# Performance work log

Measured on AMD Instinct MI355X. Metric: run time of the kernel, lower is better.

Reference implementation:

```python
import jax, jax.numpy as jnp
import numpy as np
from jax.scipy.special import ndtri

D = 1024
BITS = 4
K = 2 ** BITS
N = 4096


def _rotation_matrix(d, seed):
    # Haar-distributed random orthogonal matrix via QR with sign fix,
    # matching generate_rotation_matrix in the torch source.
    g = np.random.default_rng(seed).standard_normal((d, d)).astype(np.float32)
    Q, R = np.linalg.qr(g)
    s = np.sign(np.diag(R))
    s[s == 0] = 1.0
    return jnp.asarray((Q * s[None, :]).astype(np.float32))


def _lloyd_max_centroids(k):
    # Per-coordinate scalar codebook for a standard Gaussian (Lloyd-Max init
    # via inverse-CDF midpoints), analogous to LloydMaxCodebook.centroids [K].
    probs = (jnp.arange(k, dtype=jnp.float32) + 0.5) / k
    return ndtri(probs).astype(jnp.float32)


def setup_inputs() -> dict:
    key = jax.random.key(0)
    x = jax.random.normal(key, (N, D), dtype=jnp.float32)
    Pi = _rotation_matrix(D, seed=42)          # [d, d]
    centroids = _lloyd_max_centroids(K)        # [K]
    return {"x": x, "Pi": Pi, "centroids": centroids}


def reference(x, Pi, centroids):
    # rotate: y = x @ Pi^T
    y = x @ Pi.T                               # [N, d]
    # per-coordinate nearest-centroid argmin over K
    diffs = jnp.abs(y[..., None] - centroids)  # [N, d, K]
    indices = jnp.argmin(diffs, axis=-1)       # [N, d] int
    # dequantize: gather centroids, then unrotate x_hat = y_hat @ Pi
    y_hat = centroids[indices]                 # [N, d]
    x_hat = y_hat @ Pi                         # [N, d]
    return x_hat, indices
```

## Files before the change

### kernel.cpp

```cpp
#include <hip/hip_runtime.h>
#include <hip/hip_bf16.h>

#define TQ_D   1024
#define TQ_KC  16
#define MERGE_K 512
#define TQ_TOL  1.0e-4f
#define LCAP    1024

typedef __attribute__((ext_vector_type(8))) short bf16x8;
typedef __attribute__((ext_vector_type(4))) float f32x4;

__device__ __forceinline__ unsigned short f2bf(float f) {
    union { __hip_bfloat16 h; unsigned short s; } u;
    u.h = __float2bfloat16(f);
    return u.s;
}
__device__ __forceinline__ float bf2f(unsigned short s) {
    union { unsigned int u; float f; } v;
    v.u = (unsigned int)s << 16;
    return v.f;
}

__global__ __launch_bounds__(512)
void tq_rq_mfma(const float* __restrict__ X,
                const float* __restrict__ Pi,
                const float* __restrict__ Cent,
                float* __restrict__ OutIdx,
                unsigned* __restrict__ Counter,
                unsigned* __restrict__ List,
                unsigned cap)
{
    __shared__ unsigned short XhS[128][40];
    __shared__ unsigned short XlS[128][40];
    __shared__ unsigned short PhS[64][40];
    __shared__ unsigned short PlS[64][40];
    __shared__ unsigned lcount;
    __shared__ unsigned gbase;
    __shared__ unsigned llist[LCAP];

    const int tid  = threadIdx.x;
    const int lane = tid & 63;
    const int wv   = tid >> 6;
    const int m0 = blockIdx.y * 128;
    const int n0 = blockIdx.x * 64;
    const int wr = (wv >> 1) * 32;
    const int wc = (wv & 1) * 32;
    const int l15 = lane & 15;
    const int k8  = (lane >> 4) * 8;

    const int srow = tid >> 2;
    const int scol = (tid & 3) * 8;
    const int brow = tid >> 3;
    const int bcol = (tid & 7) * 4;

    const float* aP = X  + (size_t)(m0 + srow) * TQ_D + scol;
    const float* bP = Pi + (size_t)(n0 + brow) * TQ_D + bcol;

    if (tid == 0) lcount = 0;

    f32x4 acc[2][2];
#pragma unroll
    for (int i = 0; i < 2; ++i)
#pragma unroll
        for (int j = 0; j < 2; ++j)
#pragma unroll
            for (int r = 0; r < 4; ++r) acc[i][j][r] = 0.0f;

    float4 va[2], vb;
#pragma unroll
    for (int q = 0; q < 2; ++q) va[q] = *(const float4*)(aP + 4 * q);
    vb = *(const float4*)(bP);

#pragma unroll
    for (int q = 0; q < 2; ++q) {
        ushort4 ah, al;
        const float* fa = (const float*)&va[q];
        ah.x = f2bf(fa[0]); al.x = f2bf(fa[0] - bf2f(ah.x));
        ah.y = f2bf(fa[1]); al.y = f2bf(fa[1] - bf2f(ah.y));
        ah.z = f2bf(fa[2]); al.z = f2bf(fa[2] - bf2f(ah.z));
        ah.w = f2bf(fa[3]); al.w = f2bf(fa[3] - bf2f(ah.w));
        *(ushort4*)&XhS[srow][scol + 4 * q] = ah;
        *(ushort4*)&XlS[srow][scol + 4 * q] = al;
    }
    {
        ushort4 bh, bl;
        const float* fb = (const float*)&vb;
        bh.x = f2bf(fb[0]); bl.x = f2bf(fb[0] - bf2f(bh.x));
        bh.y = f2bf(fb[1]); bl.y = f2bf(fb[1] - bf2f(bh.y));
        bh.z = f2bf(fb[2]); bl.z = f2bf(fb[2] - bf2f(bh.z));
        bh.w = f2bf(fb[3]); bl.w = f2bf(fb[3] - bf2f(bh.w));
        *(ushort4*)&PhS[brow][bcol] = bh;
        *(ushort4*)&PlS[brow][bcol] = bl;
    }
    __syncthreads();

    for (int kt = 0; kt < 32; ++kt) {
        const bool more = (kt + 1) < 32;
        if (more) {
            const float* ap = aP + (kt + 1) * 32;
            const float* bp = bP + (kt + 1) * 32;
#pragma unroll
            for (int q = 0; q < 2; ++q) va[q] = *(const float4*)(ap + 4 * q);
            vb = *(const float4*)(bp);
        }

        bf16x8 afh[2], afl[2], bfh[2], bfl[2];
#pragma unroll
        for (int i = 0; i < 2; ++i) {
            afh[i] = *(const bf16x8*)&XhS[wr + i * 16 + l15][k8];
            afl[i] = *(const bf16x8*)&XlS[wr + i * 16 + l15][k8];
        }
#pragma unroll
        for (int j = 0; j < 2; ++j) {
            bfh[j] = *(const bf16x8*)&PhS[wc + j * 16 + l15][k8];
            bfl[j] = *(const bf16x8*)&PlS[wc + j * 16 + l15][k8];
        }

#pragma unroll
        for (int i = 0; i < 2; ++i)
#pragma unroll
            for (int j = 0; j < 2; ++j) {
                acc[i][j] = __builtin_amdgcn_mfma_f32_16x16x32_bf16(
                    afh[i], bfh[j], acc[i][j], 0, 0, 0);
                acc[i][j] = __builtin_amdgcn_mfma_f32_16x16x32_bf16(
                    afl[i], bfh[j], acc[i][j], 0, 0, 0);
                acc[i][j] = __builtin_amdgcn_mfma_f32_16x16x32_bf16(
                    afh[i], bfl[j], acc[i][j], 0, 0, 0);
                acc[i][j] = __builtin_amdgcn_mfma_f32_16x16x32_bf16(
                    afl[i], bfl[j], acc[i][j], 0, 0, 0);
            }

        if (more) {
            __syncthreads();
#pragma unroll
            for (int q = 0; q < 2; ++q) {
                ushort4 ah, al;
                const float* fa = (const float*)&va[q];
                ah.x = f2bf(fa[0]); al.x = f2bf(fa[0] - bf2f(ah.x));
                ah.y = f2bf(fa[1]); al.y = f2bf(fa[1] - bf2f(ah.y));
                ah.z = f2bf(fa[2]); al.z = f2bf(fa[2] - bf2f(ah.z));
                ah.w = f2bf(fa[3]); al.w = f2bf(fa[3] - bf2f(ah.w));
                *(ushort4*)&XhS[srow][scol + 4 * q] = ah;
                *(ushort4*)&XlS[srow][scol + 4 * q] = al;
            }
            {
                ushort4 bh, bl;
                const float* fb = (const float*)&vb;
                bh.x = f2bf(fb[0]); bl.x = f2bf(fb[0] - bf2f(bh.x));
                bh.y = f2bf(fb[1]); bl.y = f2bf(fb[1] - bf2f(bh.y));
                bh.z = f2bf(fb[2]); bl.z = f2bf(fb[2] - bf2f(bh.z));
                bh.w = f2bf(fb[3]); bl.w = f2bf(fb[3] - bf2f(bh.w));
                *(ushort4*)&PhS[brow][bcol] = bh;
                *(ushort4*)&PlS[brow][bcol] = bl;
            }
            __syncthreads();
        }
    }

    float c[TQ_KC];
#pragma unroll
    for (int q = 0; q < TQ_KC; ++q) c[q] = Cent[q];

#pragma unroll
    for (int i = 0; i < 2; ++i)
#pragma unroll
        for (int j = 0; j < 2; ++j)
#pragma unroll
            for (int r = 0; r < 4; ++r) {
                const int row = m0 + wr + i * 16 + (lane >> 4) * 4 + r;
                const int col = n0 + wc + j * 16 + l15;
                const float y = acc[i][j][r];
                int best = 0;
                float bd = fabsf(y - c[0]);
#pragma unroll
                for (int q = 1; q < TQ_KC; ++q) {
                    const float d = fabsf(y - c[q]);
                    if (d < bd) { bd = d; best = q; }
                }
                float dist = 1e30f;
#pragma unroll
                for (int q = 0; q < TQ_KC - 1; ++q) {
                    const float mid = 0.5f * (c[q] + c[q + 1]);
                    dist = fminf(dist, fabsf(y - mid));
                }
                if (dist < TQ_TOL) {
                    const unsigned id = ((unsigned)row << 10) | (unsigned)col;
                    const unsigned ls = atomicAdd(&lcount, 1u);
                    if (ls < LCAP) {
                        llist[ls] = id;
                    } else {
                        const unsigned gs = atomicAdd(Counter, 1u);
                        if (gs < cap) List[gs] = id;
                    }
                }
                OutIdx[(size_t)row * TQ_D + col] = (float)best;
            }

    __syncthreads();
    if (tid == 0) {
        const unsigned cnt = min(lcount, (unsigned)LCAP);
        gbase = (cnt > 0) ? atomicAdd(Counter, cnt) : 0u;
    }
    __syncthreads();
    const unsigned cnt = min(lcount, (unsigned)LCAP);
    for (unsigned s = tid; s < cnt; s += 512) {
        const unsigned g = gbase + s;
        if (g < cap) List[g] = llist[s];
    }
}

__global__ __launch_bounds__(256)
void tq_fixup_lds(const float* __restrict__ X,
                  const float* __restrict__ Pi,
                  const float* __restrict__ Cent,
                  float* __restrict__ OutIdx,
                  const unsigned* __restrict__ Counter,
                  const unsigned* __restrict__ List,
                  unsigned cap)
{
    __shared__ float Rows[8][2][1024];
    __shared__ float part[8][2];
    __shared__ unsigned ids[8];

    const int tid = threadIdx.x;
    const unsigned count = min(*Counter, cap);

    for (unsigned base = blockIdx.x * 8; base < count; base += gridDim.x * 8) {
        const unsigned nsus = min(8u, count - base);

        if (tid < 8) ids[tid] = (tid < nsus) ? List[base + tid] : 0u;
        __syncthreads();

#pragma unroll
        for (int q = 0; q < 16; ++q) {
            const int lin = q * 256 + tid;
            const int sus = lin >> 9;
            const int rowsel = (lin >> 8) & 1;
            const int f4 = lin & 255;
            if ((unsigned)sus < nsus) {
                const unsigned id = ids[sus];
                const int m = id >> 10;
                const int n = id & (TQ_D - 1);
                const float* src = rowsel ? (Pi + (size_t)n * TQ_D)
                                          : (X + (size_t)m * TQ_D);
                *(float4*)&Rows[sus][rowsel][f4 * 4] =
                    *(const float4*)(src + f4 * 4);
            }
        }
        __syncthreads();

        if (tid < 16 && (unsigned)(tid >> 1) < nsus) {
            const int sus = tid >> 1;
            const int p = tid & 1;
            const int kb = p * MERGE_K;
            float a = 0.0f;
            for (int k = 0; k < MERGE_K; k += 4) {
                const float4 xa = *(const float4*)&Rows[sus][0][kb + k];
                const float4 pa = *(const float4*)&Rows[sus][1][kb + k];
                a = fmaf(xa.x, pa.x, a);
                a = fmaf(xa.y, pa.y, a);
                a = fmaf(xa.z, pa.z, a);
                a = fmaf(xa.w, pa.w, a);
            }
            part[sus][p] = a;
        }
        __syncthreads();

        if (tid < (int)nsus) {
            const float y = part[tid][0] + part[tid][1];
            float c[TQ_KC];
#pragma unroll
            for (int q = 0; q < TQ_KC; ++q) c[q] = Cent[q];
            int best = 0;
            float bd = fabsf(y - c[0]);
#pragma unroll
            for (int q = 1; q < TQ_KC; ++q) {
                const float d = fabsf(y - c[q]);
                if (d < bd) { bd = d; best = q; }
            }
            const unsigned id = ids[tid];
            OutIdx[(size_t)(id >> 10) * TQ_D + (id & (TQ_D - 1))] = (float)best;
        }
        __syncthreads();
    }
}

__global__ __launch_bounds__(256)
void tq_dq_mfma(const float* __restrict__ IdxF,
                const float* __restrict__ Pi,
                const float* __restrict__ Cent,
                float* __restrict__ Xhat)
{
    __shared__ unsigned short Ys[128][40];
    __shared__ unsigned short Ps[128][40];
    __shared__ unsigned short csb[TQ_KC];

    const int tid  = threadIdx.x;
    const int lane = tid & 63;
    const int wv   = tid >> 6;
    const int m0 = blockIdx.y * 128;
    const int n0 = blockIdx.x * 128;
    const int wr = (wv >> 1) * 64;
    const int wc = (wv & 1) * 64;
    const int l15 = lane & 15;
    const int k8  = (lane >> 4) * 8;

    const int arow = tid >> 1;
    const int acol = (tid & 1) * 16;
    const int bn   = tid & 127;
    const int bkq  = (tid >> 7) * 16;

    const float* aP = IdxF + (size_t)(m0 + arow) * TQ_D + acol;
    const float* bP = Pi + (size_t)bkq * TQ_D + n0 + bn;

    if (tid < TQ_KC) csb[tid] = f2bf(Cent[tid]);

    f32x4 acc[4][4];
#pragma unroll
    for (int i = 0; i < 4; ++i)
#pragma unroll
        for (int j = 0; j < 4; ++j)
#pragma unroll
            for (int r = 0; r < 4; ++r) acc[i][j][r] = 0.0f;

    float4 va[4];
    float  vb[16];
#pragma unroll
    for (int q = 0; q < 4; ++q) va[q] = *(const float4*)(aP + 4 * q);
#pragma unroll
    for (int k = 0; k < 16; ++k) vb[k] = bP[(size_t)k * TQ_D];

    __syncthreads();

#pragma unroll
    for (int q = 0; q < 4; ++q) {
        ushort4 w;
        w.x = csb[(int)va[q].x & 15];
        w.y = csb[(int)va[q].y & 15];
        w.z = csb[(int)va[q].z & 15];
        w.w = csb[(int)va[q].w & 15];
        *(ushort4*)&Ys[arow][acol + 4 * q] = w;
    }
#pragma unroll
    for (int k = 0; k < 16; ++k) Ps[bn][bkq + k] = f2bf(vb[k]);
    __syncthreads();

    for (int kt = 0; kt < 32; ++kt) {
        const bool more = (kt + 1) < 32;
        if (more) {
            const float* ap = aP + (kt + 1) * 32;
            const float* bp = bP + (size_t)(kt + 1) * 32 * TQ_D;
#pragma unroll
            for (int q = 0; q < 4; ++q) va[q] = *(const float4*)(ap + 4 * q);
#pragma unroll
            for (int k = 0; k < 16; ++k) vb[k] = bp[(size_t)k * TQ_D];
        }

        bf16x8 af[4], bfr[4];
#pragma unroll
        for (int i = 0; i < 4; ++i)
            af[i] = *(const bf16x8*)&Ys[wr + i * 16 + l15][k8];
#pragma unroll
        for (int j = 0; j < 4; ++j)
            bfr[j] = *(const bf16x8*)&Ps[wc + j * 16 + l15][k8];

#pragma unroll
        for (int i = 0; i < 4; ++i)
#pragma unroll
            for (int j = 0; j < 4; ++j)
                acc[i][j] = __builtin_amdgcn_mfma_f32_16x16x32_bf16(
                    af[i], bfr[j], acc[i][j], 0, 0, 0);

        if (more) {
            __syncthreads();
#pragma unroll
            for (int q = 0; q < 4; ++q) {
                ushort4 w;
                w.x = csb[(int)va[q].x & 15];
                w.y = csb[(int)va[q].y & 15];
                w.z = csb[(int)va[q].z & 15];
                w.w = csb[(int)va[q].w & 15];
                *(ushort4*)&Ys[arow][acol + 4 * q] = w;
            }
#pragma unroll
            for (int k = 0; k < 16; ++k) Ps[bn][bkq + k] = f2bf(vb[k]);
            __syncthreads();
        }
    }

#pragma unroll
    for (int i = 0; i < 4; ++i)
#pragma unroll
        for (int j = 0; j < 4; ++j)
#pragma unroll
            for (int r = 0; r < 4; ++r) {
                const int row = wr + i * 16 + (lane >> 4) * 4 + r;
                const int col = wc + j * 16 + l15;
                Xhat[(size_t)(m0 + row) * TQ_D + n0 + col] = acc[i][j][r];
            }
}

extern "C" void kernel_launch(void* const* d_in, const int* in_sizes, int n_in,
                              void* d_out, int out_size, void* d_ws, size_t ws_size,
                              hipStream_t stream)
{
    const float* x    = (const float*)d_in[0];
    const float* Pi   = (const float*)d_in[1];
    const float* cent = (const float*)d_in[2];
    float* out = (float*)d_out;

    const int ND = in_sizes[0];
    const int N  = ND / TQ_D;

    float* xhat = out;
    float* oidx = out + ND;

    unsigned* counter = (unsigned*)xhat;
    unsigned* list    = (unsigned*)xhat + 16;
    const unsigned cap = (unsigned)(ND - 16);

    hipMemsetAsync(counter, 0, 4, stream);

    dim3 grid1(TQ_D / 64, N / 128);
    tq_rq_mfma<<<grid1, 512, 0, stream>>>(x, Pi, cent, oidx, counter, list, cap);

    tq_fixup_lds<<<1024, 256, 0, stream>>>(x, Pi, cent, oidx, counter, list, cap);

    dim3 grid3(TQ_D / 128, N / 128);
    tq_dq_mfma<<<grid3, 256, 0, stream>>>(oidx, Pi, cent, xhat);
}
```

Before: 123.9 us.

## Shrink dequant GEMM tile to 128x64 with 512 threads and vectorized Pi loads

The dequantize GEMM now uses 128x64 output tiles with 8 waves of 512 threads, each wave computing 32x32, and launches on the same 16x32 grid as the rotate kernel. This doubles the block count to 512 so the CUs are better covered. Pi is now read as float4 along the n dimension instead of 16 strided scalar loads per thread, and is transposed into LDS. In exchange, each loaded tile is reused less, each wave has fewer MFMAs per barrier, and the transposed LDS writes may cause bank conflicts.

```diff
diff --git a/kernel.cpp b/kernel.cpp
--- a/kernel.cpp
+++ b/kernel.cpp
@@ -285,64 +285,68 @@
     }
 }
 
-__global__ __launch_bounds__(256)
+__global__ __launch_bounds__(512)
 void tq_dq_mfma(const float* __restrict__ IdxF,
                 const float* __restrict__ Pi,
                 const float* __restrict__ Cent,
                 float* __restrict__ Xhat)
 {
     __shared__ unsigned short Ys[128][40];
-    __shared__ unsigned short Ps[128][40];
+    __shared__ unsigned short Ps[64][40];
     __shared__ unsigned short csb[TQ_KC];
 
     const int tid  = threadIdx.x;
     const int lane = tid & 63;
     const int wv   = tid >> 6;
     const int m0 = blockIdx.y * 128;
-    const int n0 = blockIdx.x * 128;
-    const int wr = (wv >> 1) * 64;
-    const int wc = (wv & 1) * 64;
+    const int n0 = blockIdx.x * 64;
+    const int wr = (wv >> 1) * 32;
+    const int wc = (wv & 1) * 32;
     const int l15 = lane & 15;
     const int k8  = (lane >> 4) * 8;
 
-    const int arow = tid >> 1;
-    const int acol = (tid & 1) * 16;
-    const int bn   = tid & 127;
-    const int bkq  = (tid >> 7) * 16;
-
-    const float* aP = IdxF + (size_t)(m0 + arow) * TQ_D + acol;
-    const float* bP = Pi + (size_t)bkq * TQ_D + n0 + bn;
+    const int srow = tid >> 2;
+    const int scol = (tid & 3) * 8;
+    const int bk = tid >> 4;
+    const int bnq = (tid & 15) * 4;
+
+    const float* aP = IdxF + (size_t)(m0 + srow) * TQ_D + scol;
+    const float* bP = Pi + (size_t)bk * TQ_D + n0 + bnq;
 
     if (tid < TQ_KC) csb[tid] = f2bf(Cent[tid]);
 
-    f32x4 acc[4][4];
-#pragma unroll
-    for (int i = 0; i < 4; ++i)
-#pragma unroll
-        for (int j = 0; j < 4; ++j)
+    f32x4 acc[2][2];
+#pragma unroll
+    for (int i = 0; i < 2; ++i)
+#pragma unroll
+        for (int j = 0; j < 2; ++j)
 #pragma unroll
             for (int r = 0; r < 4; ++r) acc[i][j][r] = 0.0f;
 
-    float4 va[4];
-    float  vb[16];
-#pragma unroll
-    for (int q = 0; q < 4; ++q) va[q] = *(const float4*)(aP + 4 * q);
-#pragma unroll
-    for (int k = 0; k < 16; ++k) vb[k] = bP[(size_t)k * TQ_D];
+    float4 va[2], vb;
+#pragma unroll
+    for (int q = 0; q < 2; ++q) va[q] = *(const float4*)(aP + 4 * q);
+    vb = *(const float4*)(bP);
 
     __syncthreads();
 
 #pragma unroll
-    for (int q = 0; q < 4; ++q) {
+    for (int q = 0; q < 2; ++q) {
         ushort4 w;
-        w.x = csb[(int)va[q].x & 15];
-        w.y = csb[(int)va[q].y & 15];
-        w.z = csb[(int)va[q].z & 15];
-        w.w = csb[(int)va[q].w & 15];
-        *(ushort4*)&Ys[arow][acol + 4 * q] = w;
-    }
-#pragma unroll
-    for (int k = 0; k < 16; ++k) Ps[bn][bkq + k] = f2bf(vb[k]);
+        const float* fa = (const float*)&va[q];
+        w.x = csb[(int)fa[0] & 15];
+        w.y = csb[(int)fa[1] & 15];
+        w.z = csb[(int)fa[2] & 15];
+        w.w = csb[(int)fa[3] & 15];
+        *(ushort4*)&Ys[srow][scol + 4 * q] = w;
+    }
+    {
+        const float* fb = (const float*)&vb;
+        Ps[bnq + 0][bk] = f2bf(fb[0]);
+        Ps[bnq + 1][bk] = f2bf(fb[1]);
+        Ps[bnq + 2][bk] = f2bf(fb[2]);
+        Ps[bnq + 3][bk] = f2bf(fb[3]);
+    }
     __syncthreads();
 
     for (int kt = 0; kt < 32; ++kt) {
@@ -351,47 +355,52 @@
             const float* ap = aP + (kt + 1) * 32;
             const float* bp = bP + (size_t)(kt + 1) * 32 * TQ_D;
 #pragma unroll
-            for (int q = 0; q < 4; ++q) va[q] = *(const float4*)(ap + 4 * q);
-#pragma unroll
-            for (int k = 0; k < 16; ++k) vb[k] = bp[(size_t)k * TQ_D];
-        }
-
-        bf16x8 af[4], bfr[4];
-#pragma unroll
-        for (int i = 0; i < 4; ++i)
+            for (int q = 0; q < 2; ++q) va[q] = *(const float4*)(ap + 4 * q);
+            vb = *(const float4*)(bp);
+        }
+
+        bf16x8 af[2], bfr[2];
+#pragma unroll
+        for (int i = 0; i < 2; ++i)
             af[i] = *(const bf16x8*)&Ys[wr + i * 16 + l15][k8];
 #pragma unroll
-        for (int j = 0; j < 4; ++j)
+        for (int j = 0; j < 2; ++j)
             bfr[j] = *(const bf16x8*)&Ps[wc + j * 16 + l15][k8];
 
 #pragma unroll
-        for (int i = 0; i < 4; ++i)
-#pragma unroll
-            for (int j = 0; j < 4; ++j)
+        for (int i = 0; i < 2; ++i)
+#pragma unroll
+            for (int j = 0; j < 2; ++j)
                 acc[i][j] = __builtin_amdgcn_mfma_f32_16x16x32_bf16(
                     af[i], bfr[j], acc[i][j], 0, 0, 0);
 
         if (more) {
             __syncthreads();
 #pragma unroll
-            for (int q = 0; q < 4; ++q) {
+            for (int q = 0; q < 2; ++q) {
                 ushort4 w;
-                w.x = csb[(int)va[q].x & 15];
-                w.y = csb[(int)va[q].y & 15];
-                w.z = csb[(int)va[q].z & 15];
-                w.w = csb[(int)va[q].w & 15];
-                *(ushort4*)&Ys[arow][acol + 4 * q] = w;
-            }
-#pragma unroll
-            for (int k = 0; k < 16; ++k) Ps[bn][bkq + k] = f2bf(vb[k]);
+                const float* fa = (const float*)&va[q];
+                w.x = csb[(int)fa[0] & 15];
+                w.y = csb[(int)fa[1] & 15];
+                w.z = csb[(int)fa[2] & 15];
+                w.w = csb[(int)fa[3] & 15];
+                *(ushort4*)&Ys[srow][scol + 4 * q] = w;
+            }
+            {
+                const float* fb = (const float*)&vb;
+                Ps[bnq + 0][bk] = f2bf(fb[0]);
+                Ps[bnq + 1][bk] = f2bf(fb[1]);
+                Ps[bnq + 2][bk] = f2bf(fb[2]);
+                Ps[bnq + 3][bk] = f2bf(fb[3]);
+            }
             __syncthreads();
         }
     }
 
 #pragma unroll
-    for (int i = 0; i < 4; ++i)
-#pragma unroll
-        for (int j = 0; j < 4; ++j)
+    for (int i = 0; i < 2; ++i)
+#pragma unroll
+        for (int j = 0; j < 2; ++j)
 #pragma unroll
             for (int r = 0; r < 4; ++r) {
                 const int row = wr + i * 16 + (lane >> 4) * 4 + r;
@@ -426,6 +435,5 @@
 
     tq_fixup_lds<<<1024, 256, 0, stream>>>(x, Pi, cent, oidx, counter, list, cap);
 
-    dim3 grid3(TQ_D / 128, N / 128);
-    tq_dq_mfma<<<grid3, 256, 0, stream>>>(oidx, Pi, cent, xhat);
-}
+    tq_dq_mfma<<<grid1, 512, 0, stream>>>(oidx, Pi, cent, xhat);
+}
```

After: 107.4 us. 1.15x faster.
